# Optimization experiments

Hardware: AMD Instinct MI355X
Metric: run time of the kernel (lower is better)

## Reference

```python
import jax, jax.numpy as jnp
import numpy as np

N = 8192          # number of nodes (dense_shape of the sparse adjacency)
E = 262144        # number of edges (nnz of the sparse tensor), avg degree 32
FLOW_ITERS = 10   # self.flow_iters


def setup_inputs() -> dict:
    key = jax.random.key(0)
    k1, k2, k3, k4 = jax.random.split(key, 4)
    rows = jax.random.randint(k1, (E,), 0, N, dtype=jnp.int32)
    cols = jax.random.randint(k2, (E,), 0, N, dtype=jnp.int32)
    values = jax.random.uniform(k3, (E,), dtype=jnp.float32)      # sparse edge weights (proportions)
    demands = jax.random.normal(k4, (N, 1), dtype=jnp.float32)    # per-node demands
    return {"values": values, "demands": demands, "rows": rows, "cols": cols}


def reference(values, demands, rows, cols):
    d = demands[:, 0]  # [N]

    def step(flow_vals, _):
        # tf.sparse.reduce_sum(flow, axis=0): sum over rows -> per-column inflow [N]
        inflow = jax.ops.segment_sum(flow_vals, cols, num_segments=N)
        # relu(inflow[:, None] - demands) -> per-node adjusted inflow [N]
        adj = jax.nn.relu(inflow - d)
        # sparse * dense with [N,1] broadcast: scale each edge by adj of its row
        return values * adj[rows], None

    flow0 = jnp.zeros_like(values)  # initial empty sparse flow == all-zero values
    flow, _ = jax.lax.scan(step, flow0, None, length=FLOW_ITERS)

    # tf.sparse.to_dense(flow)
    return jnp.zeros((N, N), dtype=values.dtype).at[rows, cols].add(flow)
```

## Files before the change

### kernel.cpp

```cpp
#include <hip/hip_runtime.h>


#define NN 8192
#define EE 262144
#define THREADS 1024
#define SORTB 64
#define EPB (EE / SORTB)
#define NB 256
#define CPB (NN / NB)
#define GROWS 32
#define NBLK 256
#define MAGIC 0x5CA1AB1Eu
#define POISON 0xAAAAAAAAu

typedef unsigned long long u64;

#define LOAD_AU(p)    __hip_atomic_load((p),  __ATOMIC_RELAXED, __HIP_MEMORY_SCOPE_AGENT)
#define STORE_AU(p,v) __hip_atomic_store((p), (v), __ATOMIC_RELAXED, __HIP_MEMORY_SCOPE_AGENT)

#define LBAR() do { asm volatile("s_waitcnt lgkmcnt(0)" ::: "memory"); \
                    __builtin_amdgcn_s_barrier(); \
                    __builtin_amdgcn_sched_barrier(0); } while (0)

union SM {
    struct { unsigned cnt[SORTB * NB]; unsigned hist[NB]; unsigned bst[NB + 1];
             unsigned offs[NB]; } so;
    struct { float acc[CPB]; float dem[CPB]; } c;
    struct { float img[2 * NN]; u64 eL[2048]; } s;
    char pad[90112];
};

__device__ __forceinline__ void flag_barrier_n(unsigned* fl, int idx, int tid, int nblk) {
    if (tid == 0) STORE_AU(&fl[idx], MAGIC);
    asm volatile("" ::: "memory");
    if (tid < 64) {
        for (;;) {
            unsigned f = (tid < nblk) ? LOAD_AU(&fl[tid]) : MAGIC;
            if (__all(f == MAGIC)) break;
            __builtin_amdgcn_s_sleep(2);
        }
    }
    asm volatile("" ::: "memory");
    __syncthreads();
}

template <int SLP>
__device__ __forceinline__ void wait_flags_n(unsigned* fl, int tid, int nblk) {
    if (tid < 64) {
        for (;;) {
            unsigned f = (tid < nblk) ? LOAD_AU(&fl[tid]) : MAGIC;
            if (__all(f == MAGIC)) break;
            __builtin_amdgcn_s_sleep(SLP);
        }
    }
    asm volatile("" ::: "memory");
    __syncthreads();
}

__device__ __forceinline__ float poll_f32(const float* p) {
    unsigned u;
    for (;;) {
        u = LOAD_AU((const unsigned*)p);
        if (u != POISON) break;
        __builtin_amdgcn_s_sleep(1);
    }
    return __uint_as_float(u);
}

__global__ void __launch_bounds__(THREADS) mega(
        const float* __restrict__ values, const float* __restrict__ dem,
        const int* __restrict__ rows, const int* __restrict__ cols,
        u64* __restrict__ se,
        u64* __restrict__ se2,
        float* __restrict__ adjF,
        float* __restrict__ adj9f,
        unsigned* __restrict__ cnt,
        unsigned* __restrict__ cnt2,
        unsigned* __restrict__ bstart,
        unsigned* __restrict__ gstart,
        unsigned* __restrict__ flagsC, unsigned* __restrict__ flagsR,
        unsigned* __restrict__ flagsE, unsigned* __restrict__ flagsR2,
        float* __restrict__ out) {
    __shared__ SM sm;
    __shared__ float a9[GROWS];
    const int bid = blockIdx.x, tid = threadIdx.x;

    if (bid < SORTB) {
        if (tid < NB) sm.so.hist[tid] = 0;
        __syncthreads();
        const int4* c4 = (const int4*)(cols + bid * EPB);
        int4 ca = c4[tid];
        atomicAdd(&sm.so.hist[ca.x >> 5], 1u);  atomicAdd(&sm.so.hist[ca.y >> 5], 1u);
        atomicAdd(&sm.so.hist[ca.z >> 5], 1u);  atomicAdd(&sm.so.hist[ca.w >> 5], 1u);
        __syncthreads();
        if (tid < NB) STORE_AU(&cnt[bid * NB + tid], sm.so.hist[tid]);
        __syncthreads();
        flag_barrier_n(flagsC, bid, tid, SORTB);

        #pragma unroll
        for (int j = 0; j < (SORTB * NB) / THREADS; ++j)
            sm.so.cnt[tid + j * THREADS] = LOAD_AU(&cnt[tid + j * THREADS]);
        __syncthreads();
        if (tid < NB) {
            unsigned t = 0;
            for (int b = 0; b < SORTB; ++b) t += sm.so.cnt[b * NB + tid];
            sm.so.hist[tid] = t;
        }
        __syncthreads();
        if (tid == 0) {
            unsigned run = 0;
            for (int k = 0; k < NB; ++k) { sm.so.bst[k] = run; run += sm.so.hist[k]; }
            sm.so.bst[NB] = run;
        }
        __syncthreads();
        if (tid < NB) {
            unsigned off = sm.so.bst[tid];
            for (int b = 0; b < bid; ++b) off += sm.so.cnt[b * NB + tid];
            sm.so.offs[tid] = off;
        }
        if (bid == 0 && tid <= NB) STORE_AU(&bstart[tid], sm.so.bst[tid]);
        __syncthreads();

        {
            const int4*   r4 = (const int4*)(rows + bid * EPB);
            const float4* v4 = (const float4*)(values + bid * EPB);
            int4 ra = r4[tid];  float4 va = v4[tid];
            #define PUSHC(R, C, V) do {                                        \
                unsigned dst_ = atomicAdd(&sm.so.offs[(C) >> 5], 1u);          \
                u64 w_ = (unsigned)((R) | (((C) & 31) << 13))                  \
                       | ((u64)__float_as_uint(V) << 32);                      \
                STORE_AU(&se[dst_], w_);                                       \
            } while (0)
            PUSHC(ra.x, ca.x, va.x);  PUSHC(ra.y, ca.y, va.y);
            PUSHC(ra.z, ca.z, va.z);  PUSHC(ra.w, ca.w, va.w);
            #undef PUSHC
        }
        __syncthreads();
        flag_barrier_n(flagsE, bid, tid, SORTB);
    } else if (bid < 2 * SORTB) {
        const int b2 = bid - SORTB;
        if (tid < NB) sm.so.hist[tid] = 0;
        __syncthreads();
        const int4* r4 = (const int4*)(rows + b2 * EPB);
        int4 ra = r4[tid];
        atomicAdd(&sm.so.hist[ra.x >> 5], 1u);  atomicAdd(&sm.so.hist[ra.y >> 5], 1u);
        atomicAdd(&sm.so.hist[ra.z >> 5], 1u);  atomicAdd(&sm.so.hist[ra.w >> 5], 1u);
        __syncthreads();
        if (tid < NB) STORE_AU(&cnt2[b2 * NB + tid], sm.so.hist[tid]);
        __syncthreads();
        flag_barrier_n(flagsR, b2, tid, SORTB);

        #pragma unroll
        for (int j = 0; j < (SORTB * NB) / THREADS; ++j)
            sm.so.cnt[tid + j * THREADS] = LOAD_AU(&cnt2[tid + j * THREADS]);
        __syncthreads();
        if (tid < NB) {
            unsigned t = 0;
            for (int b = 0; b < SORTB; ++b) t += sm.so.cnt[b * NB + tid];
            sm.so.hist[tid] = t;
        }
        __syncthreads();
        if (tid == 0) {
            unsigned run = 0;
            for (int k = 0; k < NB; ++k) { sm.so.bst[k] = run; run += sm.so.hist[k]; }
            sm.so.bst[NB] = run;
        }
        __syncthreads();
        if (tid < NB) {
            unsigned off = sm.so.bst[tid];
            for (int b = 0; b < b2; ++b) off += sm.so.cnt[b * NB + tid];
            sm.so.offs[tid] = off;
        }
        if (b2 == 0 && tid <= NB) STORE_AU(&gstart[tid], sm.so.bst[tid]);
        __syncthreads();

        {
            const int4*   c4 = (const int4*)(cols + b2 * EPB);
            const float4* v4 = (const float4*)(values + b2 * EPB);
            int4 ca = c4[tid];  float4 va = v4[tid];
            #define PUSHR(R, C, V) do {                                        \
                unsigned dst_ = atomicAdd(&sm.so.offs[(R) >> 5], 1u);          \
                u64 w_ = (unsigned)((C) | (((R) & 31) << 13))                  \
                       | ((u64)__float_as_uint(V) << 32);                      \
                STORE_AU(&se2[dst_], w_);                                      \
            } while (0)
            PUSHR(ra.x, ca.x, va.x);  PUSHR(ra.y, ca.y, va.y);
            PUSHR(ra.z, ca.z, va.z);  PUSHR(ra.w, ca.w, va.w);
            #undef PUSHR
        }
        __syncthreads();
        if (tid == 0) STORE_AU(&flagsR2[b2], MAGIC);
        asm volatile("" ::: "memory");
        wait_flags_n<4>(flagsE, tid, SORTB);
    } else {
        wait_flags_n<8>(flagsE, tid, SORTB);
    }

    const int bs = (int)LOAD_AU(&bstart[bid]);
    const int be = (int)LOAD_AU(&bstart[bid + 1]);
    const int ne = be - bs;
    u64 e0 = 0, e1 = 0;
    if (tid < ne)           e0 = LOAD_AU(&se[bs + tid]);
    if (THREADS + tid < ne) e1 = LOAD_AU(&se[bs + THREADS + tid]);
    if (tid < CPB) sm.c.dem[tid] = dem[bid * CPB + tid];

    for (int s = 1; s <= 9; ++s) {
        if (tid < CPB) sm.c.acc[tid] = 0.f;
        __syncthreads();

        #define EDGE(W) do {                                                   \
            unsigned m_ = (unsigned)(W);                                       \
            float v_ = __uint_as_float((unsigned)((W) >> 32));                 \
            int r_ = m_ & (NN - 1);                                            \
            float a_ = (s == 1) ? fmaxf(-dem[r_], 0.f)                         \
                                : poll_f32(&adjF[(size_t)(s - 1) * NN + r_]);  \
            atomicAdd(&sm.c.acc[(m_ >> 13) & 31], v_ * a_);                    \
        } while (0)
        if (tid < ne)           EDGE(e0);
        if (THREADS + tid < ne) EDGE(e1);
        for (int i = bs + 2 * THREADS + tid; i < be; i += THREADS) {
            u64 w = LOAD_AU(&se[i]);
            EDGE(w);
        }
        #undef EDGE
        __syncthreads();

        if (tid < CPB) {
            float r = fmaxf(sm.c.acc[tid] - sm.c.dem[tid], 0.f);
            if (s < 9) STORE_AU(&adjF[(size_t)s * NN + bid * CPB + tid], r);
            else       STORE_AU(&adj9f[bid * CPB + tid], r);
        }
    }
    wait_flags_n<2>(flagsR2, tid, SORTB);

    {
        const int g = bid;
        const unsigned gs = LOAD_AU(&gstart[g]), ge = LOAD_AU(&gstart[g + 1]);
        const unsigned n = ge - gs;
        const unsigned ncp = n < 2048u ? n : 2048u;
        if (tid < GROWS) a9[tid] = poll_f32(&adj9f[g * GROWS + tid]);
        __syncthreads();

        for (unsigned i = tid; i < ncp; i += THREADS) {
            u64 w = LOAD_AU(&se2[gs + i]);
            unsigned m = (unsigned)w;
            float v = __uint_as_float((unsigned)(w >> 32));
            sm.s.eL[i] = (u64)m | ((u64)__float_as_uint(v * a9[(m >> 13) & 31]) << 32);
        }
        __syncthreads();

        const float4 z4 = make_float4(0.f, 0.f, 0.f, 0.f);
        for (int r = 0; r < GROWS; ++r) {
            float* im = sm.s.img + (r & 1) * NN;
            ((float4*)im)[tid]        = z4;
            ((float4*)im)[tid + 1024] = z4;
            LBAR();
            for (unsigned i = tid; i < ncp; i += THREADS) {
                u64 w = sm.s.eL[i];
                unsigned m = (unsigned)w;
                if (((m >> 13) & 31) == (unsigned)r)
                    atomicAdd(&im[m & (NN - 1)], __uint_as_float((unsigned)(w >> 32)));
            }
            for (unsigned i = 2048u + tid; i < n; i += THREADS) {
                u64 w = LOAD_AU(&se2[gs + i]);
                unsigned m = (unsigned)w;
                if (((m >> 13) & 31) == (unsigned)r)
                    atomicAdd(&im[m & (NN - 1)],
                              __uint_as_float((unsigned)(w >> 32)) * a9[r]);
            }
            LBAR();
            float4 w0 = ((const float4*)im)[tid];
            float4 w1 = ((const float4*)im)[tid + 1024];
            float4* o4 = (float4*)(out + (size_t)(g * GROWS + r) * NN);
            o4[tid]        = w0;
            o4[tid + 1024] = w1;
        }
    }
}

extern "C" void kernel_launch(void* const* d_in, const int* in_sizes, int n_in,
                              void* d_out, int out_size, void* d_ws, size_t ws_size,
                              hipStream_t stream) {
    const float* values = (const float*)d_in[0];
    const float* dem    = (const float*)d_in[1];
    const int*   rows   = (const int*)d_in[2];
    const int*   cols   = (const int*)d_in[3];
    float* out = (float*)d_out;

    u64*      se      = (u64*)d_ws;
    u64*      se2     = se + (size_t)EE;
    float*    adjF    = (float*)(se2 + (size_t)EE);
    float*    adj9f   = adjF + 9L * NN;
    unsigned* cnt     = (unsigned*)(adj9f + NN);
    unsigned* cnt2    = cnt + SORTB * NB;
    unsigned* bstart  = cnt2 + SORTB * NB;
    unsigned* gstart  = bstart + 320;
    unsigned* flagsC  = gstart + 320;
    unsigned* flagsR  = flagsC + 64;
    unsigned* flagsE  = flagsR + 64;
    unsigned* flagsR2 = flagsE + 64;

    mega<<<NBLK, THREADS, 0, stream>>>(
        values, dem, rows, cols, se, se2, adjF, adj9f, cnt, cnt2,
        bstart, gstart, flagsC, flagsR, flagsE, flagsR2, out);
}
```

Baseline: 309.0 us.

## Replace grid flag barriers with per-element poison polling on workspace data

Removes the four grid-wide flag barriers and instead has each consumer spin on individual workspace words (counts, bucket starts, sorted edges, adj values) until they differ from a poison sentinel. Blocks can start on data as soon as that data is ready instead of waiting for every producer block. It also drops the pre-scaling pass of se2 edges (the scale is now applied in the scatter loop) and zeroes both image buffers once up front, clearing each after readback, which removes one barrier per row. This depends on the workspace being poison-filled before every launch and on no real value matching the sentinel, and per-element polling adds load and sleep overhead.

```diff
diff --git a/kernel.cpp b/kernel.cpp
--- a/kernel.cpp
+++ b/kernel.cpp
@@ -10,8 +10,8 @@
 #define CPB (NN / NB)
 #define GROWS 32
 #define NBLK 256
-#define MAGIC 0x5CA1AB1Eu
-#define POISON 0xAAAAAAAAu
+#define POISON32 0xAAAAAAAAu
+#define POISON64 0xAAAAAAAAAAAAAAAAull
 
 typedef unsigned long long u64;
 
@@ -25,43 +25,32 @@
 union SM {
     struct { unsigned cnt[SORTB * NB]; unsigned hist[NB]; unsigned bst[NB + 1];
              unsigned offs[NB]; } so;
-    struct { float acc[CPB]; float dem[CPB]; } c;
     struct { float img[2 * NN]; u64 eL[2048]; } s;
-    char pad[90112];
 };
 
-__device__ __forceinline__ void flag_barrier_n(unsigned* fl, int idx, int tid, int nblk) {
-    if (tid == 0) STORE_AU(&fl[idx], MAGIC);
-    asm volatile("" ::: "memory");
-    if (tid < 64) {
-        for (;;) {
-            unsigned f = (tid < nblk) ? LOAD_AU(&fl[tid]) : MAGIC;
-            if (__all(f == MAGIC)) break;
-            __builtin_amdgcn_s_sleep(2);
-        }
-    }
-    asm volatile("" ::: "memory");
-    __syncthreads();
-}
-
-template <int SLP>
-__device__ __forceinline__ void wait_flags_n(unsigned* fl, int tid, int nblk) {
-    if (tid < 64) {
-        for (;;) {
-            unsigned f = (tid < nblk) ? LOAD_AU(&fl[tid]) : MAGIC;
-            if (__all(f == MAGIC)) break;
-            __builtin_amdgcn_s_sleep(SLP);
-        }
-    }
-    asm volatile("" ::: "memory");
-    __syncthreads();
-}
-
+__device__ __forceinline__ unsigned poll_u32(const unsigned* p) {
+    unsigned u;
+    for (;;) {
+        u = LOAD_AU(p);
+        if (u != POISON32) break;
+        __builtin_amdgcn_s_sleep(1);
+    }
+    return u;
+}
+__device__ __forceinline__ u64 poll_u64(const u64* p) {
+    u64 w;
+    for (;;) {
+        w = LOAD_AU(p);
+        if (w != POISON64) break;
+        __builtin_amdgcn_s_sleep(1);
+    }
+    return w;
+}
 __device__ __forceinline__ float poll_f32(const float* p) {
     unsigned u;
     for (;;) {
         u = LOAD_AU((const unsigned*)p);
-        if (u != POISON) break;
+        if (u != POISON32) break;
         __builtin_amdgcn_s_sleep(1);
     }
     return __uint_as_float(u);
@@ -78,10 +67,10 @@
         unsigned* __restrict__ cnt2,
         unsigned* __restrict__ bstart,
         unsigned* __restrict__ gstart,
-        unsigned* __restrict__ flagsC, unsigned* __restrict__ flagsR,
-        unsigned* __restrict__ flagsE, unsigned* __restrict__ flagsR2,
         float* __restrict__ out) {
     __shared__ SM sm;
+    __shared__ float accL[CPB];
+    __shared__ float demL[CPB];
     __shared__ float a9[GROWS];
     const int bid = blockIdx.x, tid = threadIdx.x;
 
@@ -94,12 +83,10 @@
         atomicAdd(&sm.so.hist[ca.z >> 5], 1u);  atomicAdd(&sm.so.hist[ca.w >> 5], 1u);
         __syncthreads();
         if (tid < NB) STORE_AU(&cnt[bid * NB + tid], sm.so.hist[tid]);
-        __syncthreads();
-        flag_barrier_n(flagsC, bid, tid, SORTB);
 
         #pragma unroll
         for (int j = 0; j < (SORTB * NB) / THREADS; ++j)
-            sm.so.cnt[tid + j * THREADS] = LOAD_AU(&cnt[tid + j * THREADS]);
+            sm.so.cnt[tid + j * THREADS] = poll_u32(&cnt[tid + j * THREADS]);
         __syncthreads();
         if (tid < NB) {
             unsigned t = 0;
@@ -135,8 +122,6 @@
             PUSHC(ra.z, ca.z, va.z);  PUSHC(ra.w, ca.w, va.w);
             #undef PUSHC
         }
-        __syncthreads();
-        flag_barrier_n(flagsE, bid, tid, SORTB);
     } else if (bid < 2 * SORTB) {
         const int b2 = bid - SORTB;
         if (tid < NB) sm.so.hist[tid] = 0;
@@ -147,12 +132,10 @@
         atomicAdd(&sm.so.hist[ra.z >> 5], 1u);  atomicAdd(&sm.so.hist[ra.w >> 5], 1u);
         __syncthreads();
         if (tid < NB) STORE_AU(&cnt2[b2 * NB + tid], sm.so.hist[tid]);
-        __syncthreads();
-        flag_barrier_n(flagsR, b2, tid, SORTB);
 
         #pragma unroll
         for (int j = 0; j < (SORTB * NB) / THREADS; ++j)
-            sm.so.cnt[tid + j * THREADS] = LOAD_AU(&cnt2[tid + j * THREADS]);
+            sm.so.cnt[tid + j * THREADS] = poll_u32(&cnt2[tid + j * THREADS]);
         __syncthreads();
         if (tid < NB) {
             unsigned t = 0;
@@ -188,24 +171,18 @@
             PUSHR(ra.z, ca.z, va.z);  PUSHR(ra.w, ca.w, va.w);
             #undef PUSHR
         }
-        __syncthreads();
-        if (tid == 0) STORE_AU(&flagsR2[b2], MAGIC);
-        asm volatile("" ::: "memory");
-        wait_flags_n<4>(flagsE, tid, SORTB);
-    } else {
-        wait_flags_n<8>(flagsE, tid, SORTB);
-    }
-
-    const int bs = (int)LOAD_AU(&bstart[bid]);
-    const int be = (int)LOAD_AU(&bstart[bid + 1]);
+    }
+
+    const int bs = (int)poll_u32(&bstart[bid]);
+    const int be = (int)poll_u32(&bstart[bid + 1]);
     const int ne = be - bs;
     u64 e0 = 0, e1 = 0;
-    if (tid < ne)           e0 = LOAD_AU(&se[bs + tid]);
-    if (THREADS + tid < ne) e1 = LOAD_AU(&se[bs + THREADS + tid]);
-    if (tid < CPB) sm.c.dem[tid] = dem[bid * CPB + tid];
+    if (tid < ne)           e0 = poll_u64(&se[bs + tid]);
+    if (THREADS + tid < ne) e1 = poll_u64(&se[bs + THREADS + tid]);
+    if (tid < CPB) demL[tid] = dem[bid * CPB + tid];
 
     for (int s = 1; s <= 9; ++s) {
-        if (tid < CPB) sm.c.acc[tid] = 0.f;
+        if (tid < CPB) accL[tid] = 0.f;
         __syncthreads();
 
         #define EDGE(W) do {                                                   \
@@ -214,63 +191,62 @@
             int r_ = m_ & (NN - 1);                                            \
             float a_ = (s == 1) ? fmaxf(-dem[r_], 0.f)                         \
                                 : poll_f32(&adjF[(size_t)(s - 1) * NN + r_]);  \
-            atomicAdd(&sm.c.acc[(m_ >> 13) & 31], v_ * a_);                    \
+            atomicAdd(&accL[(m_ >> 13) & 31], v_ * a_);                        \
         } while (0)
         if (tid < ne)           EDGE(e0);
         if (THREADS + tid < ne) EDGE(e1);
         for (int i = bs + 2 * THREADS + tid; i < be; i += THREADS) {
-            u64 w = LOAD_AU(&se[i]);
+            u64 w = poll_u64(&se[i]);
             EDGE(w);
         }
         #undef EDGE
         __syncthreads();
 
         if (tid < CPB) {
-            float r = fmaxf(sm.c.acc[tid] - sm.c.dem[tid], 0.f);
+            float r = fmaxf(accL[tid] - demL[tid], 0.f);
             if (s < 9) STORE_AU(&adjF[(size_t)s * NN + bid * CPB + tid], r);
             else       STORE_AU(&adj9f[bid * CPB + tid], r);
         }
     }
-    wait_flags_n<2>(flagsR2, tid, SORTB);
 
     {
         const int g = bid;
-        const unsigned gs = LOAD_AU(&gstart[g]), ge = LOAD_AU(&gstart[g + 1]);
+        const unsigned gs = poll_u32(&gstart[g]), ge = poll_u32(&gstart[g + 1]);
         const unsigned n = ge - gs;
         const unsigned ncp = n < 2048u ? n : 2048u;
         if (tid < GROWS) a9[tid] = poll_f32(&adj9f[g * GROWS + tid]);
-        __syncthreads();
-
-        for (unsigned i = tid; i < ncp; i += THREADS) {
-            u64 w = LOAD_AU(&se2[gs + i]);
-            unsigned m = (unsigned)w;
-            float v = __uint_as_float((unsigned)(w >> 32));
-            sm.s.eL[i] = (u64)m | ((u64)__float_as_uint(v * a9[(m >> 13) & 31]) << 32);
-        }
-        __syncthreads();
+
+        for (unsigned i = tid; i < ncp; i += THREADS)
+            sm.s.eL[i] = poll_u64(&se2[gs + i]);
 
         const float4 z4 = make_float4(0.f, 0.f, 0.f, 0.f);
+        float4* iz = (float4*)sm.s.img;
+        iz[tid] = z4;  iz[tid + 1024] = z4;
+        iz[tid + 2048] = z4;  iz[tid + 3072] = z4;
+        __syncthreads();
+
         for (int r = 0; r < GROWS; ++r) {
             float* im = sm.s.img + (r & 1) * NN;
-            ((float4*)im)[tid]        = z4;
-            ((float4*)im)[tid + 1024] = z4;
-            LBAR();
+            const float ar = a9[r];
             for (unsigned i = tid; i < ncp; i += THREADS) {
                 u64 w = sm.s.eL[i];
                 unsigned m = (unsigned)w;
                 if (((m >> 13) & 31) == (unsigned)r)
-                    atomicAdd(&im[m & (NN - 1)], __uint_as_float((unsigned)(w >> 32)));
+                    atomicAdd(&im[m & (NN - 1)],
+                              __uint_as_float((unsigned)(w >> 32)) * ar);
             }
             for (unsigned i = 2048u + tid; i < n; i += THREADS) {
-                u64 w = LOAD_AU(&se2[gs + i]);
+                u64 w = poll_u64(&se2[gs + i]);
                 unsigned m = (unsigned)w;
                 if (((m >> 13) & 31) == (unsigned)r)
                     atomicAdd(&im[m & (NN - 1)],
-                              __uint_as_float((unsigned)(w >> 32)) * a9[r]);
+                              __uint_as_float((unsigned)(w >> 32)) * ar);
             }
             LBAR();
             float4 w0 = ((const float4*)im)[tid];
             float4 w1 = ((const float4*)im)[tid + 1024];
+            ((float4*)im)[tid] = z4;
+            ((float4*)im)[tid + 1024] = z4;
             float4* o4 = (float4*)(out + (size_t)(g * GROWS + r) * NN);
             o4[tid]        = w0;
             o4[tid + 1024] = w1;
@@ -295,12 +271,8 @@
     unsigned* cnt2    = cnt + SORTB * NB;
     unsigned* bstart  = cnt2 + SORTB * NB;
     unsigned* gstart  = bstart + 320;
-    unsigned* flagsC  = gstart + 320;
-    unsigned* flagsR  = flagsC + 64;
-    unsigned* flagsE  = flagsR + 64;
-    unsigned* flagsR2 = flagsE + 64;
 
     mega<<<NBLK, THREADS, 0, stream>>>(
         values, dem, rows, cols, se, se2, adjF, adj9f, cnt, cnt2,
-        bstart, gstart, flagsC, flagsR, flagsE, flagsR2, out);
-}
+        bstart, gstart, out);
+}
```

Measured after the change: 311.2 us. No clear change (+0.7%).
